# Kernel optimization log

Hardware: AMD Instinct MI355X
Metric: run time of the kernel (lower is better)

The kernel has to match this reference:

```python
import jax, jax.numpy as jnp
import numpy as np

B, D, L, E, H = 8192, 1024, 256, 16, 400

def setup_inputs() -> dict:
    key = jax.random.key(0)
    ks = jax.random.split(key, 6)
    s1 = 1.0 / np.sqrt(D)
    s2 = 1.0 / np.sqrt(H)
    return {
        "x": jax.random.normal(ks[0], (B, D), dtype=jnp.float32),
        "angle_idx": jax.random.randint(ks[1], (B,), 0, E, dtype=jnp.int64),
        "W1": jax.random.uniform(ks[2], (E, D, H), jnp.float32, -s1, s1),
        "b1": jax.random.uniform(ks[3], (E, H), jnp.float32, -s1, s1),
        "W2": jax.random.uniform(ks[4], (E, H, 2 * L), jnp.float32, -s2, s2),
        "b2": jax.random.uniform(ks[5], (E, 2 * L), jnp.float32, -s2, s2),
    }

def reference(x, angle_idx, W1, b1, W2, b2):
    # Dense all-experts compute, then per-sample select (jit-friendly MoE dispatch).
    # h1: [E, B, H]
    h1 = jax.nn.relu(jnp.einsum('bd,edh->ebh', x, W1) + b1[:, None, :])
    # h: [E, B, 2L]
    h = jnp.einsum('ebh,ehk->ebk', h1, W2) + b2[:, None, :]
    sel = h[angle_idx, jnp.arange(x.shape[0])]  # [B, 2L], each row from its routed expert
    half = sel.shape[1] // 2
    z_mu, z_logvar = sel[:, :half], sel[:, half:]
    return (z_mu, z_logvar)
```

## Files before the change

### kernel.cpp

```cpp
#include <hip/hip_runtime.h>
#include <hip/hip_bf16.h>
#include <cstdint>
#include <cstddef>

#define B_N 8192
#define D_K 1024
#define H_N 400
#define HP  416
#define K2_N 512
#define E_N 16
#define L_N 256
#define TM 64
#define PAD_ROWS (B_N + E_N * TM)
#define NTILES (PAD_ROWS / TM)

typedef short bf16x8 __attribute__((ext_vector_type(8)));
typedef float f32x4 __attribute__((ext_vector_type(4)));

static __device__ __forceinline__ unsigned short f2bf(float f) {
  union { float f; unsigned int u; } c; c.f = f;
  unsigned int u = c.u + 0x7fffu + ((c.u >> 16) & 1u);
  return (unsigned short)(u >> 16);
}
static __device__ __forceinline__ unsigned int pkbf(float a, float b) {
  union { __hip_bfloat162 v; unsigned int u; } c;
  c.v = __float22bfloat162_rn(make_float2(a, b));
  return c.u;
}

__global__ __launch_bounds__(256) void hist_kernel(const int* __restrict__ idx,
                                                   int* __restrict__ hist) {
  __shared__ int h[E_N];
  int t = threadIdx.x;
  if (t < E_N) h[t] = 0;
  __syncthreads();
  int b = blockIdx.x * 256 + t;
  atomicAdd(&h[idx[b]], 1);
  __syncthreads();
  if (t < E_N) hist[blockIdx.x * E_N + t] = h[t];
}

__global__ __launch_bounds__(256) void offs_kernel(const int* __restrict__ hist,
                                                   int* __restrict__ off_al,
                                                   int* __restrict__ cur,
                                                   int* __restrict__ order) {
  __shared__ int cnt[E_N];
  int t = threadIdx.x;
  if (t < E_N) {
    int s = 0;
    for (int b = 0; b < 32; ++b) s += hist[b * E_N + t];
    cnt[t] = s;
  }
  __syncthreads();
  if (t == 0) {
    int acc = 0;
    for (int e = 0; e < E_N; ++e) {
      off_al[e] = acc;
      cur[e] = acc;
      acc += ((cnt[e] + TM - 1) / TM) * TM;
    }
    off_al[E_N] = acc;
  }
  for (int i = t; i < PAD_ROWS; i += 256) order[i] = -1;
}

__global__ __launch_bounds__(256) void scatter_kernel(const int* __restrict__ idx,
                                                      int* __restrict__ cur,
                                                      int* __restrict__ order) {
  int b = blockIdx.x * 256 + threadIdx.x;
  int e = idx[b];
  int p = atomicAdd(&cur[e], 1);
  order[p] = b;
}

__global__ __launch_bounds__(256) void transpose_kernel(const float* __restrict__ src,
                                                        unsigned short* __restrict__ dst,
                                                        int K, int N, int Kd) {
  __shared__ unsigned short Ls[64][72];
  const int e  = blockIdx.z;
  const int k0 = blockIdx.x * 64;
  const int n0 = blockIdx.y * 64;
  const float* S = src + (size_t)e * K * N;
  unsigned short* Dt = dst + (size_t)e * N * Kd;
  const int t = threadIdx.x;
  const int kk = t >> 4;
  const int nn = (t & 15) * 4;
#pragma unroll
  for (int p = 0; p < 4; ++p) {
    int k = k0 + p * 16 + kk;
    int n = n0 + nn;
    float4 v = make_float4(0.f, 0.f, 0.f, 0.f);
    if (k < K && n + 3 < N) v = *(const float4*)(S + (size_t)k * N + n);
    Ls[nn + 0][p * 16 + kk] = f2bf(v.x);
    Ls[nn + 1][p * 16 + kk] = f2bf(v.y);
    Ls[nn + 2][p * 16 + kk] = f2bf(v.z);
    Ls[nn + 3][p * 16 + kk] = f2bf(v.w);
  }
  __syncthreads();
  const int n2 = t >> 3;
  const int ch = t & 7;
#pragma unroll
  for (int p = 0; p < 2; ++p) {
    int n = n0 + p * 32 + n2;
    int k = k0 + ch * 8;
    if (n < N && k < Kd)
      *(uint4*)(Dt + (size_t)n * Kd + k) = *(const uint4*)&Ls[p * 32 + n2][ch * 8];
  }
}

__global__ __launch_bounds__(256) void gemm1_kernel(const float* __restrict__ x,
                                                    const unsigned short* __restrict__ Wt1,
                                                    const float* __restrict__ b1,
                                                    const int* __restrict__ off_al,
                                                    const int* __restrict__ order,
                                                    unsigned short* __restrict__ h1buf) {
  __shared__ int offs[E_N + 1];
  __shared__ int rowidx[TM];
  __shared__ unsigned short As[64 * 40];
  __shared__ unsigned short Bs[112 * 40];
  const int tid = threadIdx.x;
  const int m0 = blockIdx.x * TM;
  const int nb = blockIdx.y;
  const int tstart = (nb < 2) ? 7 * nb : 14 + 6 * (nb - 2);
  const int tcnt   = (nb < 2) ? 7 : 6;
  const int nbase  = tstart * 16;
  if (tid <= E_N) offs[tid] = off_al[tid];
  if (tid < TM) rowidx[tid] = order[m0 + tid];
  __syncthreads();
  const int total = offs[E_N];
  if (m0 >= total) return;
  int e = 0;
  while (m0 >= offs[e + 1]) ++e;

  const int arow = tid >> 2;
  const int akq  = (tid & 3) * 8;
  const long asrc = rowidx[arow];
  const unsigned short* Wt1e = Wt1 + (size_t)e * H_N * D_K;

  const int lane = tid & 63, w = tid >> 6;
  const int ln = lane & 15, q = lane >> 4;
  const int nload = tcnt * 64;

  const int i0 = tid, i1 = tid + 256;
  const int br0 = i0 >> 2, bc0 = (i0 & 3) * 8;
  const int br1 = i1 >> 2, bc1 = (i1 & 3) * 8;
  const int bg0 = nbase + br0, bg1 = nbase + br1;
  const bool v1 = (i1 < nload) && (bg1 < H_N);
  const bool v0 = (bg0 < H_N);

  f32x4 acc[4][2] = {};

  float4 aA = make_float4(0, 0, 0, 0), aB = aA;
  if (asrc >= 0) {
    aA = *(const float4*)(x + (size_t)asrc * D_K + akq);
    aB = *(const float4*)(x + (size_t)asrc * D_K + akq + 4);
  }
  uint4 breg0 = make_uint4(0, 0, 0, 0), breg1 = breg0;
  if (v0) breg0 = *(const uint4*)(Wt1e + (size_t)bg0 * D_K + bc0);
  if (v1) breg1 = *(const uint4*)(Wt1e + (size_t)bg1 * D_K + bc1);

  for (int k0 = 0; k0 < D_K; k0 += 32) {
    uint4 aw;
    aw.x = pkbf(aA.x, aA.y); aw.y = pkbf(aA.z, aA.w);
    aw.z = pkbf(aB.x, aB.y); aw.w = pkbf(aB.z, aB.w);
    *(uint4*)&As[arow * 40 + akq] = aw;
    *(uint4*)&Bs[br0 * 40 + bc0] = breg0;
    if (i1 < nload) *(uint4*)&Bs[br1 * 40 + bc1] = breg1;
    __syncthreads();

    int kn = k0 + 32;
    if (kn < D_K) {
      if (asrc >= 0) {
        aA = *(const float4*)(x + (size_t)asrc * D_K + kn + akq);
        aB = *(const float4*)(x + (size_t)asrc * D_K + kn + akq + 4);
      }
      if (v0) breg0 = *(const uint4*)(Wt1e + (size_t)bg0 * D_K + kn + bc0);
      if (v1) breg1 = *(const uint4*)(Wt1e + (size_t)bg1 * D_K + kn + bc1);
    }

    bf16x8 af[4];
#pragma unroll
    for (int i = 0; i < 4; ++i)
      af[i] = *(const bf16x8*)&As[(16 * i + ln) * 40 + 8 * q];
#pragma unroll
    for (int t = 0; t < 2; ++t) {
      int tl = w + 4 * t;
      if (tl < tcnt) {
        bf16x8 bfrag = *(const bf16x8*)&Bs[(16 * tl + ln) * 40 + 8 * q];
#pragma unroll
        for (int i = 0; i < 4; ++i)
          acc[i][t] = __builtin_amdgcn_mfma_f32_16x16x32_bf16(af[i], bfrag, acc[i][t], 0, 0, 0);
      }
    }
    __syncthreads();
  }

#pragma unroll
  for (int t = 0; t < 2; ++t) {
    int tl = w + 4 * t;
    if (tl < tcnt) {
      int n = nbase + 16 * tl + ln;
      if (n < H_N) {
        float bias = b1[e * H_N + n];
#pragma unroll
        for (int i = 0; i < 4; ++i) {
#pragma unroll
          for (int r = 0; r < 4; ++r) {
            int m = m0 + 16 * i + 4 * q + r;
            float v = acc[i][t][r] + bias;
            h1buf[(size_t)m * HP + n] = f2bf(fmaxf(v, 0.f));
          }
        }
      }
    }
  }
  if (nb == 3 && tid < TM) {
    uint4 z = make_uint4(0, 0, 0, 0);
    *(uint4*)&h1buf[(size_t)(m0 + tid) * HP + 400] = z;
    *(uint4*)&h1buf[(size_t)(m0 + tid) * HP + 408] = z;
  }
}

__global__ __launch_bounds__(256) void gemm2_kernel(const unsigned short* __restrict__ h1buf,
                                                    const unsigned short* __restrict__ Wt2,
                                                    const float* __restrict__ b2,
                                                    const int* __restrict__ off_al,
                                                    const int* __restrict__ order,
                                                    float* __restrict__ out) {
  __shared__ int offs[E_N + 1];
  __shared__ int rowidx[TM];
  __shared__ unsigned short As[64 * 40];
  __shared__ unsigned short Bs[128 * 40];
  const int tid = threadIdx.x;
  const int m0 = blockIdx.x * TM;
  const int nb = blockIdx.y;
  const int nbase = nb * 128;
  if (tid <= E_N) offs[tid] = off_al[tid];
  if (tid < TM) rowidx[tid] = order[m0 + tid];
  __syncthreads();
  const int total = offs[E_N];
  if (m0 >= total) return;
  int e = 0;
  while (m0 >= offs[e + 1]) ++e;

  const int arow = tid >> 2, ach = (tid & 3) * 8;
  const unsigned short* Wt2e = Wt2 + (size_t)e * K2_N * HP;

  const int lane = tid & 63, w = tid >> 6;
  const int ln = lane & 15, q = lane >> 4;

  const int i0 = tid, i1 = tid + 256;
  const int br0 = i0 >> 2, bc0 = (i0 & 3) * 8;
  const int br1 = i1 >> 2, bc1 = (i1 & 3) * 8;

  f32x4 acc[4][2] = {};

  uint4 areg = *(const uint4*)(h1buf + (size_t)(m0 + arow) * HP + ach);
  uint4 breg0 = *(const uint4*)(Wt2e + (size_t)(nbase + br0) * HP + bc0);
  uint4 breg1 = *(const uint4*)(Wt2e + (size_t)(nbase + br1) * HP + bc1);

  for (int k0 = 0; k0 < HP; k0 += 32) {
    *(uint4*)&As[arow * 40 + ach] = areg;
    *(uint4*)&Bs[br0 * 40 + bc0] = breg0;
    *(uint4*)&Bs[br1 * 40 + bc1] = breg1;
    __syncthreads();

    int kn = k0 + 32;
    if (kn < HP) {
      areg  = *(const uint4*)(h1buf + (size_t)(m0 + arow) * HP + kn + ach);
      breg0 = *(const uint4*)(Wt2e + (size_t)(nbase + br0) * HP + kn + bc0);
      breg1 = *(const uint4*)(Wt2e + (size_t)(nbase + br1) * HP + kn + bc1);
    }

    bf16x8 af[4];
#pragma unroll
    for (int i = 0; i < 4; ++i)
      af[i] = *(const bf16x8*)&As[(16 * i + ln) * 40 + 8 * q];
#pragma unroll
    for (int t = 0; t < 2; ++t) {
      int tl = w + 4 * t;
      bf16x8 bfrag = *(const bf16x8*)&Bs[(16 * tl + ln) * 40 + 8 * q];
#pragma unroll
      for (int i = 0; i < 4; ++i)
        acc[i][t] = __builtin_amdgcn_mfma_f32_16x16x32_bf16(af[i], bfrag, acc[i][t], 0, 0, 0);
    }
    __syncthreads();
  }

#pragma unroll
  for (int t = 0; t < 2; ++t) {
    int tl = w + 4 * t;
    int n = nbase + 16 * tl + ln;
    float bias = b2[e * K2_N + n];
#pragma unroll
    for (int i = 0; i < 4; ++i) {
#pragma unroll
      for (int r = 0; r < 4; ++r) {
        int s = rowidx[16 * i + 4 * q + r];
        if (s >= 0) {
          float v = acc[i][t][r] + bias;
          if (n < L_N) out[(size_t)s * L_N + n] = v;
          else         out[(size_t)(B_N + s) * L_N + (n - L_N)] = v;
        }
      }
    }
  }
}

extern "C" void kernel_launch(void* const* d_in, const int* in_sizes, int n_in,
                              void* d_out, int out_size, void* d_ws, size_t ws_size,
                              hipStream_t stream) {
  const float* x   = (const float*)d_in[0];
  const int*   idx = (const int*)d_in[1];
  const float* W1  = (const float*)d_in[2];
  const float* b1  = (const float*)d_in[3];
  const float* W2  = (const float*)d_in[4];
  const float* b2  = (const float*)d_in[5];
  float* out = (float*)d_out;

  char* ws = (char*)d_ws;
  int* off_al = (int*)(ws + 0);
  int* cur    = (int*)(ws + 128);
  int* hist   = (int*)(ws + 192);
  int* order  = (int*)(ws + 2240);
  unsigned short* h1buf = (unsigned short*)(ws + 39104);
  unsigned short* Wt1   = (unsigned short*)(ws + 7706816);
  unsigned short* Wt2   = Wt1;

  hist_kernel<<<32, 256, 0, stream>>>(idx, hist);
  offs_kernel<<<1, 256, 0, stream>>>(hist, off_al, cur, order);
  scatter_kernel<<<32, 256, 0, stream>>>(idx, cur, order);
  transpose_kernel<<<dim3(D_K / 64, 7, E_N), 256, 0, stream>>>(W1, Wt1, D_K, H_N, D_K);
  gemm1_kernel<<<dim3(NTILES, 4), 256, 0, stream>>>(x, Wt1, b1, off_al, order, h1buf);
  transpose_kernel<<<dim3(HP / 64 + 1, K2_N / 64, E_N), 256, 0, stream>>>(W2, Wt2, H_N, K2_N, HP);
  gemm2_kernel<<<dim3(NTILES, 4), 256, 0, stream>>>(h1buf, Wt2, b2, off_al, order, out);
}
```

Baseline: 194.8 us.

## Merge prep kernels, pre-gather x to bf16, use async LDS loads with swizzled double buffering

```diff
diff --git a/kernel.cpp b/kernel.cpp
--- a/kernel.cpp
+++ b/kernel.cpp
@@ -17,6 +17,10 @@
 typedef short bf16x8 __attribute__((ext_vector_type(8)));
 typedef float f32x4 __attribute__((ext_vector_type(4)));
 
+#define GLDS(gp, lp) __builtin_amdgcn_global_load_lds( \
+    (const __attribute__((address_space(1))) unsigned int*)(gp), \
+    (__attribute__((address_space(3))) unsigned int*)(lp), 16, 0, 0)
+
 static __device__ __forceinline__ unsigned short f2bf(float f) {
   union { float f; unsigned int u; } c; c.f = f;
   unsigned int u = c.u + 0x7fffu + ((c.u >> 16) & 1u);
@@ -28,189 +32,178 @@
   return c.u;
 }
 
-__global__ __launch_bounds__(256) void hist_kernel(const int* __restrict__ idx,
-                                                   int* __restrict__ hist) {
-  __shared__ int h[E_N];
-  int t = threadIdx.x;
-  if (t < E_N) h[t] = 0;
-  __syncthreads();
-  int b = blockIdx.x * 256 + t;
-  atomicAdd(&h[idx[b]], 1);
-  __syncthreads();
-  if (t < E_N) hist[blockIdx.x * E_N + t] = h[t];
-}
-
-__global__ __launch_bounds__(256) void offs_kernel(const int* __restrict__ hist,
+__global__ __launch_bounds__(256) void prep_kernel(const float* __restrict__ W1,
+                                                   const float* __restrict__ W2,
+                                                   const int* __restrict__ idx,
+                                                   unsigned short* __restrict__ Wt1,
+                                                   unsigned short* __restrict__ Wt2,
                                                    int* __restrict__ off_al,
-                                                   int* __restrict__ cur,
                                                    int* __restrict__ order) {
-  __shared__ int cnt[E_N];
-  int t = threadIdx.x;
-  if (t < E_N) {
-    int s = 0;
-    for (int b = 0; b < 32; ++b) s += hist[b * E_N + t];
-    cnt[t] = s;
-  }
-  __syncthreads();
-  if (t == 0) {
-    int acc = 0;
-    for (int e = 0; e < E_N; ++e) {
-      off_al[e] = acc;
-      cur[e] = acc;
-      acc += ((cnt[e] + TM - 1) / TM) * TM;
-    }
-    off_al[E_N] = acc;
-  }
-  for (int i = t; i < PAD_ROWS; i += 256) order[i] = -1;
-}
-
-__global__ __launch_bounds__(256) void scatter_kernel(const int* __restrict__ idx,
-                                                      int* __restrict__ cur,
-                                                      int* __restrict__ order) {
-  int b = blockIdx.x * 256 + threadIdx.x;
-  int e = idx[b];
-  int p = atomicAdd(&cur[e], 1);
-  order[p] = b;
-}
-
-__global__ __launch_bounds__(256) void transpose_kernel(const float* __restrict__ src,
-                                                        unsigned short* __restrict__ dst,
-                                                        int K, int N, int Kd) {
-  __shared__ unsigned short Ls[64][72];
-  const int e  = blockIdx.z;
-  const int k0 = blockIdx.x * 64;
-  const int n0 = blockIdx.y * 64;
-  const float* S = src + (size_t)e * K * N;
-  unsigned short* Dt = dst + (size_t)e * N * Kd;
+  const int bid = blockIdx.x;
   const int t = threadIdx.x;
-  const int kk = t >> 4;
-  const int nn = (t & 15) * 4;
-#pragma unroll
-  for (int p = 0; p < 4; ++p) {
-    int k = k0 + p * 16 + kk;
-    int n = n0 + nn;
-    float4 v = make_float4(0.f, 0.f, 0.f, 0.f);
-    if (k < K && n + 3 < N) v = *(const float4*)(S + (size_t)k * N + n);
-    Ls[nn + 0][p * 16 + kk] = f2bf(v.x);
-    Ls[nn + 1][p * 16 + kk] = f2bf(v.y);
-    Ls[nn + 2][p * 16 + kk] = f2bf(v.z);
-    Ls[nn + 3][p * 16 + kk] = f2bf(v.w);
-  }
-  __syncthreads();
-  const int n2 = t >> 3;
-  const int ch = t & 7;
-#pragma unroll
-  for (int p = 0; p < 2; ++p) {
-    int n = n0 + p * 32 + n2;
-    int k = k0 + ch * 8;
-    if (n < N && k < Kd)
-      *(uint4*)(Dt + (size_t)n * Kd + k) = *(const uint4*)&Ls[p * 32 + n2][ch * 8];
-  }
-}
-
-__global__ __launch_bounds__(256) void gemm1_kernel(const float* __restrict__ x,
+  if (bid < 2688) {
+    __shared__ unsigned short Ls[64][72];
+    const float* S; unsigned short* Dt; int K, N, Kd, Nd, k0, n0;
+    if (bid < 1792) {
+      int e = bid / 112, r = bid % 112;
+      k0 = (r % 16) * 64; n0 = (r / 16) * 64;
+      S = W1 + (size_t)e * D_K * H_N; Dt = Wt1 + (size_t)e * HP * D_K;
+      K = D_K; N = H_N; Kd = D_K; Nd = HP;
+    } else {
+      int t2 = bid - 1792; int e = t2 / 56, r = t2 % 56;
+      k0 = (r % 7) * 64; n0 = (r / 7) * 64;
+      S = W2 + (size_t)e * H_N * K2_N; Dt = Wt2 + (size_t)e * K2_N * HP;
+      K = H_N; N = K2_N; Kd = HP; Nd = K2_N;
+    }
+    const int kk = t >> 4;
+    const int nn = (t & 15) * 4;
+#pragma unroll
+    for (int p = 0; p < 4; ++p) {
+      int k = k0 + p * 16 + kk;
+      int n = n0 + nn;
+      float4 v = make_float4(0.f, 0.f, 0.f, 0.f);
+      if (k < K && n + 3 < N) v = *(const float4*)(S + (size_t)k * N + n);
+      Ls[nn + 0][p * 16 + kk] = f2bf(v.x);
+      Ls[nn + 1][p * 16 + kk] = f2bf(v.y);
+      Ls[nn + 2][p * 16 + kk] = f2bf(v.z);
+      Ls[nn + 3][p * 16 + kk] = f2bf(v.w);
+    }
+    __syncthreads();
+    const int n2 = t >> 3;
+    const int ch = t & 7;
+#pragma unroll
+    for (int p = 0; p < 2; ++p) {
+      int n = n0 + p * 32 + n2;
+      int k = k0 + ch * 8;
+      if (n < Nd && k < Kd)
+        *(uint4*)(Dt + (size_t)n * Kd + k) = *(const uint4*)&Ls[p * 32 + n2][ch * 8];
+    }
+  } else {
+    __shared__ int cnt[E_N];
+    __shared__ int curS[E_N];
+    if (t < E_N) cnt[t] = 0;
+    __syncthreads();
+    for (int b = t; b < B_N; b += 256) atomicAdd(&cnt[idx[b]], 1);
+    __syncthreads();
+    if (t == 0) {
+      int acc = 0;
+      for (int e = 0; e < E_N; ++e) {
+        off_al[e] = acc; curS[e] = acc;
+        acc += ((cnt[e] + TM - 1) / TM) * TM;
+      }
+      off_al[E_N] = acc;
+    }
+    for (int i = t; i < PAD_ROWS; i += 256) order[i] = -1;
+    __syncthreads();
+    for (int b = t; b < B_N; b += 256) {
+      int e = idx[b];
+      order[atomicAdd(&curS[e], 1)] = b;
+    }
+  }
+}
+
+__global__ __launch_bounds__(256) void gather_x_kernel(const float* __restrict__ x,
+                                                       const int* __restrict__ order,
+                                                       unsigned short* __restrict__ xg) {
+  const int w = threadIdx.x >> 6, l = threadIdx.x & 63;
+  const int row = blockIdx.x * 4 + w;
+  const int src = order[row];
+  unsigned short* dst = xg + (size_t)row * D_K;
+  if (src < 0) {
+#pragma unroll
+    for (int i = 0; i < 4; ++i)
+      *(uint2*)(dst + i * 256 + l * 4) = make_uint2(0, 0);
+  } else {
+    const float* s = x + (size_t)src * D_K;
+#pragma unroll
+    for (int i = 0; i < 4; ++i) {
+      float4 v = *(const float4*)(s + i * 256 + l * 4);
+      uint2 o; o.x = pkbf(v.x, v.y); o.y = pkbf(v.z, v.w);
+      *(uint2*)(dst + i * 256 + l * 4) = o;
+    }
+  }
+}
+
+__global__ __launch_bounds__(256) void gemm1_kernel(const unsigned short* __restrict__ xg,
                                                     const unsigned short* __restrict__ Wt1,
                                                     const float* __restrict__ b1,
                                                     const int* __restrict__ off_al,
-                                                    const int* __restrict__ order,
                                                     unsigned short* __restrict__ h1buf) {
+  __shared__ unsigned short As[2][64 * 32];
+  __shared__ unsigned short Bs[2][112 * 32];
   __shared__ int offs[E_N + 1];
-  __shared__ int rowidx[TM];
-  __shared__ unsigned short As[64 * 40];
-  __shared__ unsigned short Bs[112 * 40];
   const int tid = threadIdx.x;
   const int m0 = blockIdx.x * TM;
   const int nb = blockIdx.y;
   const int tstart = (nb < 2) ? 7 * nb : 14 + 6 * (nb - 2);
   const int tcnt   = (nb < 2) ? 7 : 6;
-  const int nbase  = tstart * 16;
   if (tid <= E_N) offs[tid] = off_al[tid];
-  if (tid < TM) rowidx[tid] = order[m0 + tid];
   __syncthreads();
-  const int total = offs[E_N];
-  if (m0 >= total) return;
+  if (m0 >= offs[E_N]) return;
   int e = 0;
   while (m0 >= offs[e + 1]) ++e;
-
-  const int arow = tid >> 2;
-  const int akq  = (tid & 3) * 8;
-  const long asrc = rowidx[arow];
-  const unsigned short* Wt1e = Wt1 + (size_t)e * H_N * D_K;
-
-  const int lane = tid & 63, w = tid >> 6;
-  const int ln = lane & 15, q = lane >> 4;
-  const int nload = tcnt * 64;
-
-  const int i0 = tid, i1 = tid + 256;
-  const int br0 = i0 >> 2, bc0 = (i0 & 3) * 8;
-  const int br1 = i1 >> 2, bc1 = (i1 & 3) * 8;
-  const int bg0 = nbase + br0, bg1 = nbase + br1;
-  const bool v1 = (i1 < nload) && (bg1 < H_N);
-  const bool v0 = (bg0 < H_N);
+  const unsigned short* Wt1e = Wt1 + (size_t)e * HP * D_K;
+
+  const int l = tid & 63, w = tid >> 6;
+  const int r4 = l >> 2;
+  const int sg = (r4 ^ (r4 >> 2)) & 3;
+  const int g8 = ((l & 3) ^ sg) * 8;
+  const int tl1 = w + 4;
+  const unsigned short* gA  = xg + (size_t)(m0 + 16 * w + r4) * D_K + g8;
+  const unsigned short* gB0 = Wt1e + (size_t)((tstart + w) * 16 + r4) * D_K + g8;
+  const unsigned short* gB1 = Wt1e + (size_t)((tstart + tl1) * 16 + r4) * D_K + g8;
+
+  const int ln = l & 15, q = l >> 4;
+  const int sr = (ln ^ (ln >> 2)) & 3;
+  const int cq = (q ^ sr) * 8;
 
   f32x4 acc[4][2] = {};
 
-  float4 aA = make_float4(0, 0, 0, 0), aB = aA;
-  if (asrc >= 0) {
-    aA = *(const float4*)(x + (size_t)asrc * D_K + akq);
-    aB = *(const float4*)(x + (size_t)asrc * D_K + akq + 4);
-  }
-  uint4 breg0 = make_uint4(0, 0, 0, 0), breg1 = breg0;
-  if (v0) breg0 = *(const uint4*)(Wt1e + (size_t)bg0 * D_K + bc0);
-  if (v1) breg1 = *(const uint4*)(Wt1e + (size_t)bg1 * D_K + bc1);
+  GLDS(gA, &As[0][16 * w * 32]);
+  GLDS(gB0, &Bs[0][16 * w * 32]);
+  if (tl1 < tcnt) GLDS(gB1, &Bs[0][16 * tl1 * 32]);
 
   for (int k0 = 0; k0 < D_K; k0 += 32) {
-    uint4 aw;
-    aw.x = pkbf(aA.x, aA.y); aw.y = pkbf(aA.z, aA.w);
-    aw.z = pkbf(aB.x, aB.y); aw.w = pkbf(aB.z, aB.w);
-    *(uint4*)&As[arow * 40 + akq] = aw;
-    *(uint4*)&Bs[br0 * 40 + bc0] = breg0;
-    if (i1 < nload) *(uint4*)&Bs[br1 * 40 + bc1] = breg1;
-    __syncthreads();
-
-    int kn = k0 + 32;
-    if (kn < D_K) {
-      if (asrc >= 0) {
-        aA = *(const float4*)(x + (size_t)asrc * D_K + kn + akq);
-        aB = *(const float4*)(x + (size_t)asrc * D_K + kn + akq + 4);
-      }
-      if (v0) breg0 = *(const uint4*)(Wt1e + (size_t)bg0 * D_K + kn + bc0);
-      if (v1) breg1 = *(const uint4*)(Wt1e + (size_t)bg1 * D_K + kn + bc1);
-    }
-
+    const int cur = (k0 >> 5) & 1;
+    const int nxt = cur ^ 1;
+    __syncthreads();
+    if (k0 + 32 < D_K) {
+      GLDS(gA + k0 + 32, &As[nxt][16 * w * 32]);
+      GLDS(gB0 + k0 + 32, &Bs[nxt][16 * w * 32]);
+      if (tl1 < tcnt) GLDS(gB1 + k0 + 32, &Bs[nxt][16 * tl1 * 32]);
+    }
     bf16x8 af[4];
 #pragma unroll
     for (int i = 0; i < 4; ++i)
-      af[i] = *(const bf16x8*)&As[(16 * i + ln) * 40 + 8 * q];
-#pragma unroll
-    for (int t = 0; t < 2; ++t) {
-      int tl = w + 4 * t;
-      if (tl < tcnt) {
-        bf16x8 bfrag = *(const bf16x8*)&Bs[(16 * tl + ln) * 40 + 8 * q];
+      af[i] = *(const bf16x8*)&As[cur][(16 * i + ln) * 32 + cq];
+    {
+      bf16x8 bf0 = *(const bf16x8*)&Bs[cur][(16 * w + ln) * 32 + cq];
+#pragma unroll
+      for (int i = 0; i < 4; ++i)
+        acc[i][0] = __builtin_amdgcn_mfma_f32_16x16x32_bf16(af[i], bf0, acc[i][0], 0, 0, 0);
+    }
+    if (tl1 < tcnt) {
+      bf16x8 bf1 = *(const bf16x8*)&Bs[cur][(16 * tl1 + ln) * 32 + cq];
+#pragma unroll
+      for (int i = 0; i < 4; ++i)
+        acc[i][1] = __builtin_amdgcn_mfma_f32_16x16x32_bf16(af[i], bf1, acc[i][1], 0, 0, 0);
+    }
+  }
+
+#pragma unroll
+  for (int t = 0; t < 2; ++t) {
+    const int tl = w + 4 * t;
+    if (tl < tcnt) {
+      const int n = (tstart + tl) * 16 + ln;
+      if (n < H_N) {
+        const float bias = b1[e * H_N + n];
 #pragma unroll
         for (int i = 0; i < 4; ++i)
-          acc[i][t] = __builtin_amdgcn_mfma_f32_16x16x32_bf16(af[i], bfrag, acc[i][t], 0, 0, 0);
-      }
-    }
-    __syncthreads();
-  }
-
-#pragma unroll
-  for (int t = 0; t < 2; ++t) {
-    int tl = w + 4 * t;
-    if (tl < tcnt) {
-      int n = nbase + 16 * tl + ln;
-      if (n < H_N) {
-        float bias = b1[e * H_N + n];
-#pragma unroll
-        for (int i = 0; i < 4; ++i) {
 #pragma unroll
           for (int r = 0; r < 4; ++r) {
-            int m = m0 + 16 * i + 4 * q + r;
-            float v = acc[i][t][r] + bias;
-            h1buf[(size_t)m * HP + n] = f2bf(fmaxf(v, 0.f));
+            const int m = m0 + 16 * i + 4 * q + r;
+            h1buf[(size_t)m * HP + n] = f2bf(fmaxf(acc[i][t][r] + bias, 0.f));
           }
-        }
       }
     }
   }
@@ -227,83 +220,79 @@
                                                     const int* __restrict__ off_al,
                                                     const int* __restrict__ order,
                                                     float* __restrict__ out) {
+  __shared__ unsigned short As[2][64 * 32];
+  __shared__ unsigned short Bs[2][128 * 32];
   __shared__ int offs[E_N + 1];
   __shared__ int rowidx[TM];
-  __shared__ unsigned short As[64 * 40];
-  __shared__ unsigned short Bs[128 * 40];
   const int tid = threadIdx.x;
   const int m0 = blockIdx.x * TM;
-  const int nb = blockIdx.y;
-  const int nbase = nb * 128;
+  const int nbase = blockIdx.y * 128;
   if (tid <= E_N) offs[tid] = off_al[tid];
   if (tid < TM) rowidx[tid] = order[m0 + tid];
   __syncthreads();
-  const int total = offs[E_N];
-  if (m0 >= total) return;
+  if (m0 >= offs[E_N]) return;
   int e = 0;
   while (m0 >= offs[e + 1]) ++e;
-
-  const int arow = tid >> 2, ach = (tid & 3) * 8;
   const unsigned short* Wt2e = Wt2 + (size_t)e * K2_N * HP;
 
-  const int lane = tid & 63, w = tid >> 6;
-  const int ln = lane & 15, q = lane >> 4;
-
-  const int i0 = tid, i1 = tid + 256;
-  const int br0 = i0 >> 2, bc0 = (i0 & 3) * 8;
-  const int br1 = i1 >> 2, bc1 = (i1 & 3) * 8;
+  const int l = tid & 63, w = tid >> 6;
+  const int r4 = l >> 2;
+  const int sg = (r4 ^ (r4 >> 2)) & 3;
+  const int g8 = ((l & 3) ^ sg) * 8;
+  const int tl1 = w + 4;
+  const unsigned short* gA  = h1buf + (size_t)(m0 + 16 * w + r4) * HP + g8;
+  const unsigned short* gB0 = Wt2e + (size_t)(nbase + 16 * w + r4) * HP + g8;
+  const unsigned short* gB1 = Wt2e + (size_t)(nbase + 16 * tl1 + r4) * HP + g8;
+
+  const int ln = l & 15, q = l >> 4;
+  const int sr = (ln ^ (ln >> 2)) & 3;
+  const int cq = (q ^ sr) * 8;
 
   f32x4 acc[4][2] = {};
 
-  uint4 areg = *(const uint4*)(h1buf + (size_t)(m0 + arow) * HP + ach);
-  uint4 breg0 = *(const uint4*)(Wt2e + (size_t)(nbase + br0) * HP + bc0);
-  uint4 breg1 = *(const uint4*)(Wt2e + (size_t)(nbase + br1) * HP + bc1);
+  GLDS(gA, &As[0][16 * w * 32]);
+  GLDS(gB0, &Bs[0][16 * w * 32]);
+  GLDS(gB1, &Bs[0][16 * tl1 * 32]);
 
   for (int k0 = 0; k0 < HP; k0 += 32) {
-    *(uint4*)&As[arow * 40 + ach] = areg;
-    *(uint4*)&Bs[br0 * 40 + bc0] = breg0;
-    *(uint4*)&Bs[br1 * 40 + bc1] = breg1;
-    __syncthreads();
-
-    int kn = k0 + 32;
-    if (kn < HP) {
-      areg  = *(const uint4*)(h1buf + (size_t)(m0 + arow) * HP + kn + ach);
-      breg0 = *(const uint4*)(Wt2e + (size_t)(nbase + br0) * HP + kn + bc0);
-      breg1 = *(const uint4*)(Wt2e + (size_t)(nbase + br1) * HP + kn + bc1);
-    }
-
+    const int cur = (k0 >> 5) & 1;
+    const int nxt = cur ^ 1;
+    __syncthreads();
+    if (k0 + 32 < HP) {
+      GLDS(gA + k0 + 32, &As[nxt][16 * w * 32]);
+      GLDS(gB0 + k0 + 32, &Bs[nxt][16 * w * 32]);
+      GLDS(gB1 + k0 + 32, &Bs[nxt][16 * tl1 * 32]);
+    }
     bf16x8 af[4];
 #pragma unroll
     for (int i = 0; i < 4; ++i)
-      af[i] = *(const bf16x8*)&As[(16 * i + ln) * 40 + 8 * q];
+      af[i] = *(const bf16x8*)&As[cur][(16 * i + ln) * 32 + cq];
 #pragma unroll
     for (int t = 0; t < 2; ++t) {
-      int tl = w + 4 * t;
-      bf16x8 bfrag = *(const bf16x8*)&Bs[(16 * tl + ln) * 40 + 8 * q];
+      const int tl = w + 4 * t;
+      bf16x8 bfr = *(const bf16x8*)&Bs[cur][(16 * tl + ln) * 32 + cq];
 #pragma unroll
       for (int i = 0; i < 4; ++i)
-        acc[i][t] = __builtin_amdgcn_mfma_f32_16x16x32_bf16(af[i], bfrag, acc[i][t], 0, 0, 0);
-    }
-    __syncthreads();
+        acc[i][t] = __builtin_amdgcn_mfma_f32_16x16x32_bf16(af[i], bfr, acc[i][t], 0, 0, 0);
+    }
   }
 
 #pragma unroll
   for (int t = 0; t < 2; ++t) {
-    int tl = w + 4 * t;
-    int n = nbase + 16 * tl + ln;
-    float bias = b2[e * K2_N + n];
-#pragma unroll
-    for (int i = 0; i < 4; ++i) {
+    const int tl = w + 4 * t;
+    const int n = nbase + 16 * tl + ln;
+    const float bias = b2[e * K2_N + n];
+#pragma unroll
+    for (int i = 0; i < 4; ++i)
 #pragma unroll
       for (int r = 0; r < 4; ++r) {
-        int s = rowidx[16 * i + 4 * q + r];
+        const int s = rowidx[16 * i + 4 * q + r];
         if (s >= 0) {
-          float v = acc[i][t][r] + bias;
+          const float v = acc[i][t][r] + bias;
           if (n < L_N) out[(size_t)s * L_N + n] = v;
           else         out[(size_t)(B_N + s) * L_N + (n - L_N)] = v;
         }
       }
-    }
   }
 }
 
@@ -320,18 +309,14 @@
 
   char* ws = (char*)d_ws;
   int* off_al = (int*)(ws + 0);
-  int* cur    = (int*)(ws + 128);
-  int* hist   = (int*)(ws + 192);
   int* order  = (int*)(ws + 2240);
-  unsigned short* h1buf = (unsigned short*)(ws + 39104);
-  unsigned short* Wt1   = (unsigned short*)(ws + 7706816);
-  unsigned short* Wt2   = Wt1;
-
-  hist_kernel<<<32, 256, 0, stream>>>(idx, hist);
-  offs_kernel<<<1, 256, 0, stream>>>(hist, off_al, cur, order);
-  scatter_kernel<<<32, 256, 0, stream>>>(idx, cur, order);
-  transpose_kernel<<<dim3(D_K / 64, 7, E_N), 256, 0, stream>>>(W1, Wt1, D_K, H_N, D_K);
-  gemm1_kernel<<<dim3(NTILES, 4), 256, 0, stream>>>(x, Wt1, b1, off_al, order, h1buf);
-  transpose_kernel<<<dim3(HP / 64 + 1, K2_N / 64, E_N), 256, 0, stream>>>(W2, Wt2, H_N, K2_N, HP);
-  gemm2_kernel<<<dim3(NTILES, 4), 256, 0, stream>>>(h1buf, Wt2, b2, off_al, order, out);
-}
+  unsigned short* xg  = (unsigned short*)(ws + 39104);
+  unsigned short* h1  = (unsigned short*)(ws + 18913472);
+  unsigned short* Wt1 = (unsigned short*)(ws + 26581184);
+  unsigned short* Wt2 = (unsigned short*)(ws + 40212672);
+
+  prep_kernel<<<2689, 256, 0, stream>>>(W1, W2, idx, Wt1, Wt2, off_al, order);
+  gather_x_kernel<<<PAD_ROWS / 4, 256, 0, stream>>>(x, order, xg);
+  gemm1_kernel<<<dim3(NTILES, 4), 256, 0, stream>>>(xg, Wt1, b1, off_al, h1);
+  gemm2_kernel<<<dim3(NTILES, 4), 256, 0, stream>>>(h1, Wt2, b2, off_al, order, out);
+}
```

New measurement: 179.3 us. 7.9% less time.
